# Optimization experiments

Hardware: AMD Instinct MI355X
Metric: run time of the kernel (lower is better)

Reference implementation:

```python
import jax, jax.numpy as jnp
import numpy as np

D_MODEL = 1024
D_STATE = 128


def setup_inputs() -> dict:
    key = jax.random.key(0)
    ks = jax.random.split(key, 16)
    dm, ds = D_MODEL, D_STATE
    def lin(kw, kb, out_f, in_f):
        # torch nn.Linear default init: U(-1/sqrt(in), 1/sqrt(in))
        bound = 1.0 / np.sqrt(in_f)
        W = jax.random.uniform(kw, (out_f, in_f), jnp.float32, -bound, bound)
        b = jax.random.uniform(kb, (out_f,), jnp.float32, -bound, bound)
        return W, b
    x = jax.random.normal(ks[0], (8, 2048, dm), jnp.float32)
    A = jax.random.normal(ks[1], (ds, ds), jnp.float32) * 0.05  # scaled for stability of the recurrence
    B_w, B_b = lin(ks[2], ks[3], ds, dm)
    C_w, C_b = lin(ks[4], ks[5], dm, ds)
    D_w, D_b = lin(ks[6], ks[7], dm, dm)
    s_w1, s_b1 = lin(ks[8], ks[9], dm // 2, dm)
    s_w2, s_b2 = lin(ks[10], ks[11], ds, dm // 2)
    g_w, g_b = lin(ks[12], ks[13], dm, dm)
    return {"x": x, "A": A, "B_w": B_w, "B_b": B_b, "C_w": C_w, "C_b": C_b,
            "D_w": D_w, "D_b": D_b, "s_w1": s_w1, "s_b1": s_b1,
            "s_w2": s_w2, "s_b2": s_b2, "g_w": g_w, "g_b": g_b}


def reference(x, A, B_w, B_b, C_w, C_b, D_w, D_b, s_w1, s_b1, s_w2, s_b2, g_w, g_b):
    # Precompute all per-timestep input projections as batched GEMMs.
    s = jax.nn.sigmoid(jax.nn.silu(jnp.einsum('btd,hd->bth', x, s_w1) + s_b1)
                       @ s_w2.T + s_b2)            # [B,T,d_state] selection gate
    Bt = jnp.einsum('btd,sd->bts', x, B_w) + B_b    # [B,T,d_state]
    u = Bt * s                                      # driving input to the recurrence

    # Linear recurrence h_t = h_{t-1} @ A.T + u_t via lax.scan over time.
    h0 = jnp.zeros((x.shape[0], A.shape[0]), x.dtype)
    def step(h, u_t):
        h = h @ A.T + u_t
        return h, h
    _, hs = jax.lax.scan(step, h0, jnp.swapaxes(u, 0, 1))  # [T,B,d_state]
    hs = jnp.swapaxes(hs, 0, 1)                            # [B,T,d_state]

    y = jnp.einsum('bts,ds->btd', hs, C_w) + C_b + jnp.einsum('btd,ed->bte', x, D_w) + D_b
    gate = jax.nn.sigmoid(jnp.einsum('btd,ed->bte', x, g_w) + g_b)
    return y * gate
```

## Files before the change

kernel.cpp:

```cpp
#include <hip/hip_runtime.h>
#include <hip/hip_bf16.h>

typedef __bf16 bf16x8 __attribute__((ext_vector_type(8)));
typedef float f32x4 __attribute__((ext_vector_type(4)));

#define M_TOK 16384
#define CHUNK 64
#define NCHUNK 32

__device__ __forceinline__ void gload16(const void* g, void* l) {
    __builtin_amdgcn_global_load_lds(
        (const __attribute__((address_space(1))) void*)g,
        (__attribute__((address_space(3))) void*)l, 16, 0, 0);
}

__device__ __forceinline__ float sigmoidf_(float v) { return 1.f / (1.f + __expf(-v)); }

__global__ __launch_bounds__(256) void f32_to_bf16_k(const float* __restrict__ in,
                                                     __hip_bfloat16* __restrict__ out, int n8) {
    int i = blockIdx.x * 256 + threadIdx.x;
    if (i >= n8) return;
    const f32x4* p4 = reinterpret_cast<const f32x4*>(in) + (size_t)i * 2;
    f32x4 a = p4[0], b = p4[1];
    union { __hip_bfloat16 h[8]; uint4 u; } o;
    o.h[0] = __float2bfloat16(a[0]); o.h[1] = __float2bfloat16(a[1]);
    o.h[2] = __float2bfloat16(a[2]); o.h[3] = __float2bfloat16(a[3]);
    o.h[4] = __float2bfloat16(b[0]); o.h[5] = __float2bfloat16(b[1]);
    o.h[6] = __float2bfloat16(b[2]); o.h[7] = __float2bfloat16(b[3]);
    *reinterpret_cast<uint4*>(out + (size_t)i * 8) = o.u;
}

__global__ __launch_bounds__(256)
void wconv6(const float* s0, const float* s1, const float* s2, const float* s3,
            const float* s4, const float* s5,
            __hip_bfloat16* d0, __hip_bfloat16* d1, __hip_bfloat16* d2,
            __hip_bfloat16* d3, __hip_bfloat16* d4, __hip_bfloat16* d5,
            int n0, int n1, int n2, int n3, int n4, int n5) {
    const float* src; __hip_bfloat16* dst; int n8;
    switch (blockIdx.y) {
        case 0: src = s0; dst = d0; n8 = n0; break;
        case 1: src = s1; dst = d1; n8 = n1; break;
        case 2: src = s2; dst = d2; n8 = n2; break;
        case 3: src = s3; dst = d3; n8 = n3; break;
        case 4: src = s4; dst = d4; n8 = n4; break;
        default: src = s5; dst = d5; n8 = n5; break;
    }
    int i = blockIdx.x * 256 + threadIdx.x;
    if (i >= n8) return;
    const f32x4* p4 = reinterpret_cast<const f32x4*>(src) + (size_t)i * 2;
    f32x4 a = p4[0], b = p4[1];
    union { __hip_bfloat16 h[8]; uint4 u; } o;
    o.h[0] = __float2bfloat16(a[0]); o.h[1] = __float2bfloat16(a[1]);
    o.h[2] = __float2bfloat16(a[2]); o.h[3] = __float2bfloat16(a[3]);
    o.h[4] = __float2bfloat16(b[0]); o.h[5] = __float2bfloat16(b[1]);
    o.h[6] = __float2bfloat16(b[2]); o.h[7] = __float2bfloat16(b[3]);
    *reinterpret_cast<uint4*>(dst + (size_t)i * 8) = o.u;
}

__device__ __forceinline__ void stage128(const __hip_bfloat16* src, int ldk, size_t row0,
                                         int k0, char* lds, int tid) {
    #pragma unroll
    for (int j = 0; j < 4; ++j) {
        int q = tid + 256 * j;
        int row = q >> 3, c8 = q & 7;
        int cb = (c8 * 16) ^ ((row & 7) << 4);
        gload16((const char*)(src + (row0 + row) * (size_t)ldk + k0) + cb, lds + q * 16);
    }
}

template<int MODE>
__global__ __launch_bounds__(256, 2)
void gemm128(const __hip_bfloat16* __restrict__ X, const __hip_bfloat16* __restrict__ W,
             const __hip_bfloat16* __restrict__ Gw, const __hip_bfloat16* __restrict__ HS,
             const __hip_bfloat16* __restrict__ CW,
             const float* __restrict__ bias, const float* __restrict__ bias2,
             const float* __restrict__ biasG,
             float* __restrict__ outF, __hip_bfloat16* __restrict__ outB) {
    constexpr int N = (MODE == 0) ? 512 : 1024;
    constexpr int nN = N / 128;
    __shared__ __align__(16) char Xs[16384];
    __shared__ __align__(16) char Ws[16384];
    __shared__ __align__(16) char Gs[(MODE == 1) ? 16384 : 16];

    const int nwg  = gridDim.x;
    const int orig = blockIdx.x;
    const int v    = (orig & 7) * (nwg >> 3) + (orig >> 3);
    const size_t m0 = (size_t)(v / nN) * 128;
    const int    n0 = (v % nN) * 128;
    const int tid = threadIdx.x, lane = tid & 63, wid = tid >> 6;
    const int wm = wid >> 1, wn = wid & 1;
    const int lr = lane & 15, lg = lane >> 4;

    auto frag = [&](const char* base, int R, int kk) -> bf16x8 {
        int cb = (kk * 64 + lg * 16) ^ ((R & 7) << 4);
        return *reinterpret_cast<const bf16x8*>(base + R * 128 + cb);
    };

    f32x4 accY[4][4] = {};
    f32x4 accG[(MODE == 1) ? 4 : 1][4] = {};

    for (int k0 = 0; k0 < 1024; k0 += 64) {
        __syncthreads();
        stage128(X, 1024, m0, k0, Xs, tid);
        stage128(W, 1024, (size_t)n0, k0, Ws, tid);
        if constexpr (MODE == 1) stage128(Gw, 1024, (size_t)n0, k0, Gs, tid);
        __syncthreads();
        #pragma unroll
        for (int kk = 0; kk < 2; ++kk) {
            bf16x8 af[4];
            #pragma unroll
            for (int m = 0; m < 4; ++m) af[m] = frag(Xs, wm*64 + m*16 + lr, kk);
            #pragma unroll
            for (int n = 0; n < 4; ++n) {
                bf16x8 bw = frag(Ws, wn*64 + n*16 + lr, kk);
                #pragma unroll
                for (int m = 0; m < 4; ++m)
                    accY[m][n] = __builtin_amdgcn_mfma_f32_16x16x32_bf16(af[m], bw, accY[m][n], 0, 0, 0);
                if constexpr (MODE == 1) {
                    bf16x8 bg = frag(Gs, wn*64 + n*16 + lr, kk);
                    #pragma unroll
                    for (int m = 0; m < 4; ++m)
                        accG[m][n] = __builtin_amdgcn_mfma_f32_16x16x32_bf16(af[m], bg, accG[m][n], 0, 0, 0);
                }
            }
        }
    }
    if constexpr (MODE == 1) {
        for (int k0 = 0; k0 < 128; k0 += 64) {
            __syncthreads();
            stage128(HS, 128, m0, k0, Xs, tid);
            stage128(CW, 128, (size_t)n0, k0, Ws, tid);
            __syncthreads();
            #pragma unroll
            for (int kk = 0; kk < 2; ++kk) {
                bf16x8 af[4];
                #pragma unroll
                for (int m = 0; m < 4; ++m) af[m] = frag(Xs, wm*64 + m*16 + lr, kk);
                #pragma unroll
                for (int n = 0; n < 4; ++n) {
                    bf16x8 bw = frag(Ws, wn*64 + n*16 + lr, kk);
                    #pragma unroll
                    for (int m = 0; m < 4; ++m)
                        accY[m][n] = __builtin_amdgcn_mfma_f32_16x16x32_bf16(af[m], bw, accY[m][n], 0, 0, 0);
                }
            }
        }
    }

    #pragma unroll
    for (int m = 0; m < 4; ++m)
        #pragma unroll
        for (int n = 0; n < 4; ++n)
            #pragma unroll
            for (int rr = 0; rr < 4; ++rr) {
                size_t row = m0 + wm*64 + m*16 + lg*4 + rr;
                int col = n0 + wn*64 + n*16 + lr;
                if constexpr (MODE == 0) {
                    float vv = accY[m][n][rr] + bias[col];
                    outB[row * N + col] = __float2bfloat16(vv * sigmoidf_(vv));
                } else {
                    float y = accY[m][n][rr] + bias[col] + bias2[col];
                    float g = accG[m][n][rr] + biasG[col];
                    outF[row * 1024 + col] = y * sigmoidf_(g);
                }
            }
}

__global__ __launch_bounds__(256)
void gemm_u(const __hip_bfloat16* __restrict__ Z1, const __hip_bfloat16* __restrict__ W2,
            const float* __restrict__ b2,
            const __hip_bfloat16* __restrict__ X, const __hip_bfloat16* __restrict__ Bw,
            const float* __restrict__ Bb, __hip_bfloat16* __restrict__ U) {
    __shared__ __align__(16) char As[64 * 128];
    __shared__ __align__(16) char Bs[128 * 128];
    const int orig = blockIdx.x;
    const int v = (orig & 7) * 32 + (orig >> 3);
    const int m0 = v * 64;
    const int tid = threadIdx.x;
    const int wid = tid >> 6, lane = tid & 63;
    const int wm = wid >> 1, wn = wid & 1;
    const int lr = lane & 15, lg = lane >> 4;
    const int srow = tid >> 3, sc8 = tid & 7;

    auto fragA = [&](int R, int kk) -> bf16x8 {
        int cb = (kk * 64 + lg * 16) ^ ((R & 7) << 4);
        return *reinterpret_cast<const bf16x8*>(As + R * 128 + cb);
    };
    auto fragB = [&](int R, int kk) -> bf16x8 {
        int cb = (kk * 64 + lg * 16) ^ ((R & 7) << 4);
        return *reinterpret_cast<const bf16x8*>(Bs + R * 128 + cb);
    };

    f32x4 accS[2][4] = {};
    for (int k0 = 0; k0 < 512; k0 += 64) {
        __syncthreads();
        #pragma unroll
        for (int j = 0; j < 2; ++j) {
            int row = srow + j * 32, q = tid + 256 * j;
            int cb = (sc8 * 16) ^ ((row & 7) << 4);
            gload16((const char*)&Z1[(size_t)(m0 + row) * 512 + k0] + cb, As + q * 16);
        }
        #pragma unroll
        for (int j = 0; j < 4; ++j) {
            int row = srow + j * 32, q = tid + 256 * j;
            int cb = (sc8 * 16) ^ ((row & 7) << 4);
            gload16((const char*)&W2[(size_t)row * 512 + k0] + cb, Bs + q * 16);
        }
        __syncthreads();
        #pragma unroll
        for (int kk = 0; kk < 2; ++kk) {
            bf16x8 af[2], bfr[4];
            #pragma unroll
            for (int m = 0; m < 2; ++m) af[m] = fragA(wm*32 + m*16 + lr, kk);
            #pragma unroll
            for (int n = 0; n < 4; ++n) bfr[n] = fragB(wn*64 + n*16 + lr, kk);
            #pragma unroll
            for (int m = 0; m < 2; ++m)
                #pragma unroll
                for (int n = 0; n < 4; ++n)
                    accS[m][n] = __builtin_amdgcn_mfma_f32_16x16x32_bf16(af[m], bfr[n], accS[m][n], 0, 0, 0);
        }
    }
    #pragma unroll
    for (int m = 0; m < 2; ++m)
        #pragma unroll
        for (int n = 0; n < 4; ++n)
            #pragma unroll
            for (int r = 0; r < 4; ++r) {
                int col = wn*64 + n*16 + lr;
                accS[m][n][r] = sigmoidf_(accS[m][n][r] + b2[col]);
            }
    f32x4 accU[2][4] = {};
    for (int k0 = 0; k0 < 1024; k0 += 64) {
        __syncthreads();
        #pragma unroll
        for (int j = 0; j < 2; ++j) {
            int row = srow + j * 32, q = tid + 256 * j;
            int cb = (sc8 * 16) ^ ((row & 7) << 4);
            gload16((const char*)&X[(size_t)(m0 + row) * 1024 + k0] + cb, As + q * 16);
        }
        #pragma unroll
        for (int j = 0; j < 4; ++j) {
            int row = srow + j * 32, q = tid + 256 * j;
            int cb = (sc8 * 16) ^ ((row & 7) << 4);
            gload16((const char*)&Bw[(size_t)row * 1024 + k0] + cb, Bs + q * 16);
        }
        __syncthreads();
        #pragma unroll
        for (int kk = 0; kk < 2; ++kk) {
            bf16x8 af[2], bfr[4];
            #pragma unroll
            for (int m = 0; m < 2; ++m) af[m] = fragA(wm*32 + m*16 + lr, kk);
            #pragma unroll
            for (int n = 0; n < 4; ++n) bfr[n] = fragB(wn*64 + n*16 + lr, kk);
            #pragma unroll
            for (int m = 0; m < 2; ++m)
                #pragma unroll
                for (int n = 0; n < 4; ++n)
                    accU[m][n] = __builtin_amdgcn_mfma_f32_16x16x32_bf16(af[m], bfr[n], accU[m][n], 0, 0, 0);
        }
    }
    #pragma unroll
    for (int m = 0; m < 2; ++m)
        #pragma unroll
        for (int n = 0; n < 4; ++n)
            #pragma unroll
            for (int r = 0; r < 4; ++r) {
                int row = m0 + wm*32 + m*16 + lg*4 + r;
                int col = wn*64 + n*16 + lr;
                float uval = (accU[m][n][r] + Bb[col]) * accS[m][n][r];
                U[(size_t)row * 128 + col] = __float2bfloat16(uval);
            }
}

__global__ __launch_bounds__(128) void matpow8(const float* __restrict__ P,
                                               float* __restrict__ O) {
    __shared__ float Pl[128 * 132];
    __shared__ __align__(16) float v[2][128];
    const int tid = threadIdx.x, j = blockIdx.x;
    #pragma unroll 8
    for (int r = 0; r < 128; ++r) Pl[r * 132 + tid] = P[r * 128 + tid];
    v[0][tid] = P[tid * 128 + j];
    __syncthreads();
    int cur = 0;
    for (int it = 0; it < 7; ++it) {
        const f32x4* row = reinterpret_cast<const f32x4*>(&Pl[tid * 132]);
        const f32x4* hv  = reinterpret_cast<const f32x4*>(v[cur]);
        f32x4 s4 = {0.f, 0.f, 0.f, 0.f};
        #pragma unroll
        for (int k = 0; k < 32; ++k) s4 += row[k] * hv[k];
        v[cur ^ 1][tid] = s4[0] + s4[1] + s4[2] + s4[3];
        __syncthreads();
        cur ^= 1;
    }
    O[tid * 128 + j] = v[cur][tid];
}

__global__ __launch_bounds__(128) void ssm_phase1(const float* __restrict__ A,
                                                  const __hip_bfloat16* __restrict__ u,
                                                  float* __restrict__ E) {
    __shared__ float Al[128 * 132];
    __shared__ __align__(16) float hbuf[2][128];
    const int tid = threadIdx.x;
    #pragma unroll 8
    for (int r = 0; r < 128; ++r) Al[r * 132 + tid] = A[r * 128 + tid];
    hbuf[0][tid] = 0.f;
    __syncthreads();
    const int b = blockIdx.x >> 5, c = blockIdx.x & 31;
    const __hip_bfloat16* up = u + ((size_t)b * 2048 + c * CHUNK) * 128;
    const f32x4* Arow = reinterpret_cast<const f32x4*>(&Al[tid * 132]);
    int cur = 0;
    for (int t = 0; t < CHUNK; ++t) {
        const f32x4* hv = reinterpret_cast<const f32x4*>(hbuf[cur]);
        f32x4 s4 = {0.f, 0.f, 0.f, 0.f};
        #pragma unroll
        for (int k = 0; k < 32; ++k) s4 += Arow[k] * hv[k];
        float val = s4[0] + s4[1] + s4[2] + s4[3] + __bfloat162float(up[t * 128 + tid]);
        hbuf[cur ^ 1][tid] = val;
        __syncthreads();
        cur ^= 1;
    }
    E[(size_t)blockIdx.x * 128 + tid] = hbuf[cur][tid];
}

__global__ __launch_bounds__(128) void ssm_phase2(const float* __restrict__ A64,
                                                  const float* __restrict__ E,
                                                  float* __restrict__ starts) {
    __shared__ float Al[128 * 132];
    __shared__ __align__(16) float st[2][128];
    const int tid = threadIdx.x;
    const int b = blockIdx.x;
    #pragma unroll 8
    for (int r = 0; r < 128; ++r) Al[r * 132 + tid] = A64[r * 128 + tid];
    st[0][tid] = 0.f;
    __syncthreads();
    const f32x4* Arow = reinterpret_cast<const f32x4*>(&Al[tid * 132]);
    int cur = 0;
    for (int c = 0; c < NCHUNK; ++c) {
        starts[((size_t)b * NCHUNK + c) * 128 + tid] = st[cur][tid];
        const f32x4* hv = reinterpret_cast<const f32x4*>(st[cur]);
        f32x4 s4 = {0.f, 0.f, 0.f, 0.f};
        #pragma unroll
        for (int k = 0; k < 32; ++k) s4 += Arow[k] * hv[k];
        float val = s4[0] + s4[1] + s4[2] + s4[3] + E[((size_t)b * NCHUNK + c) * 128 + tid];
        st[cur ^ 1][tid] = val;
        __syncthreads();
        cur ^= 1;
    }
}

__global__ __launch_bounds__(128) void ssm_phase3(const float* __restrict__ A,
                                                  const __hip_bfloat16* __restrict__ u,
                                                  const float* __restrict__ starts,
                                                  __hip_bfloat16* __restrict__ hs) {
    __shared__ float Al[128 * 132];
    __shared__ __align__(16) float hbuf[2][128];
    const int tid = threadIdx.x;
    #pragma unroll 8
    for (int r = 0; r < 128; ++r) Al[r * 132 + tid] = A[r * 128 + tid];
    hbuf[0][tid] = starts[(size_t)blockIdx.x * 128 + tid];
    __syncthreads();
    const int b = blockIdx.x >> 5, c = blockIdx.x & 31;
    const size_t tok0 = (size_t)b * 2048 + c * CHUNK;
    const __hip_bfloat16* up = u + tok0 * 128;
    const f32x4* Arow = reinterpret_cast<const f32x4*>(&Al[tid * 132]);
    int cur = 0;
    for (int t = 0; t < CHUNK; ++t) {
        const f32x4* hv = reinterpret_cast<const f32x4*>(hbuf[cur]);
        f32x4 s4 = {0.f, 0.f, 0.f, 0.f};
        #pragma unroll
        for (int k = 0; k < 32; ++k) s4 += Arow[k] * hv[k];
        float val = s4[0] + s4[1] + s4[2] + s4[3] + __bfloat162float(up[t * 128 + tid]);
        hs[(tok0 + t) * 128 + tid] = __float2bfloat16(val);
        hbuf[cur ^ 1][tid] = val;
        __syncthreads();
        cur ^= 1;
    }
}

extern "C" void kernel_launch(void* const* d_in, const int* in_sizes, int n_in,
                              void* d_out, int out_size, void* d_ws, size_t ws_size,
                              hipStream_t stream) {
    const float* x    = (const float*)d_in[0];
    const float* A    = (const float*)d_in[1];
    const float* B_w  = (const float*)d_in[2];
    const float* B_b  = (const float*)d_in[3];
    const float* C_w  = (const float*)d_in[4];
    const float* C_b  = (const float*)d_in[5];
    const float* D_w  = (const float*)d_in[6];
    const float* D_b  = (const float*)d_in[7];
    const float* s_w1 = (const float*)d_in[8];
    const float* s_b1 = (const float*)d_in[9];
    const float* s_w2 = (const float*)d_in[10];
    const float* s_b2 = (const float*)d_in[11];
    const float* g_w  = (const float*)d_in[12];
    const float* g_b  = (const float*)d_in[13];
    float* out = (float*)d_out;

    char* p = (char*)d_ws;
    auto alloc = [&](size_t n) { char* r = p; p += (n + 255) & ~(size_t)255; return r; };
    __hip_bfloat16* xb    = (__hip_bfloat16*)alloc((size_t)M_TOK * 1024 * 2);
    __hip_bfloat16* w1b   = (__hip_bfloat16*)alloc(512 * 1024 * 2);
    __hip_bfloat16* w2b   = (__hip_bfloat16*)alloc(128 * 512 * 2);
    __hip_bfloat16* Bwb   = (__hip_bfloat16*)alloc(128 * 1024 * 2);
    __hip_bfloat16* Cwb   = (__hip_bfloat16*)alloc(1024 * 128 * 2);
    __hip_bfloat16* Dwb   = (__hip_bfloat16*)alloc(1024 * 1024 * 2);
    __hip_bfloat16* gwb   = (__hip_bfloat16*)alloc(1024 * 1024 * 2);
    __hip_bfloat16* z1b   = (__hip_bfloat16*)alloc((size_t)M_TOK * 512 * 2);
    __hip_bfloat16* ub    = (__hip_bfloat16*)alloc((size_t)M_TOK * 128 * 2);
    __hip_bfloat16* hsb   = (__hip_bfloat16*)alloc((size_t)M_TOK * 128 * 2);
    float* pa       = (float*)alloc(128 * 128 * 4);
    float* pb       = (float*)alloc(128 * 128 * 4);
    float* Ebuf     = (float*)alloc(256 * 128 * 4);
    float* startbuf = (float*)alloc(256 * 128 * 4);

    matpow8<<<128, 128, 0, stream>>>(A,  pa);
    matpow8<<<128, 128, 0, stream>>>(pa, pb);

    f32_to_bf16_k<<<dim3((M_TOK * 1024 / 8 + 255) / 256), dim3(256), 0, stream>>>(
        x, xb, M_TOK * 1024 / 8);
    wconv6<<<dim3(512, 6), dim3(256), 0, stream>>>(
        s_w1, s_w2, B_w, C_w, D_w, g_w,
        w1b, w2b, Bwb, Cwb, Dwb, gwb,
        512 * 1024 / 8, 128 * 512 / 8, 128 * 1024 / 8, 1024 * 128 / 8,
        1024 * 1024 / 8, 1024 * 1024 / 8);

    gemm128<0><<<dim3(512), dim3(256), 0, stream>>>(
        xb, w1b, nullptr, nullptr, nullptr, s_b1, nullptr, nullptr, nullptr, z1b);
    gemm_u<<<dim3(256), dim3(256), 0, stream>>>(z1b, w2b, s_b2, xb, Bwb, B_b, ub);

    ssm_phase1<<<256, 128, 0, stream>>>(A, ub, Ebuf);
    ssm_phase2<<<8, 128, 0, stream>>>(pb, Ebuf, startbuf);
    ssm_phase3<<<256, 128, 0, stream>>>(A, ub, startbuf, hsb);

    gemm128<1><<<dim3(1024), dim3(256), 0, stream>>>(
        xb, Dwb, gwb, hsb, Cwb, D_b, C_b, g_b, out, nullptr);
}
```

Measured before the change: 239.4 us.

## Keep transition matrix rows in registers and prefetch chunk inputs into LDS

Each thread of the scan, state-passing and matrix-power kernels now holds its row of A in 128 VGPRs instead of re-reading it from a padded LDS copy every step. The chunk's u inputs (or E values) are bulk-prefetched into LDS up front rather than loaded from global memory on every timestep. The dot product is also split into four independent accumulators to shorten the serial FMA dependency chain. The costs are very high register pressure (launch_bounds 128,1) and a slightly different summation order.

```diff
diff --git a/kernel.cpp b/kernel.cpp
--- a/kernel.cpp
+++ b/kernel.cpp
@@ -273,106 +273,138 @@
             }
 }
 
-__global__ __launch_bounds__(128) void matpow8(const float* __restrict__ P,
-                                               float* __restrict__ O) {
-    __shared__ float Pl[128 * 132];
+__global__ __launch_bounds__(128, 1) void matpow8(const float* __restrict__ P,
+                                                  float* __restrict__ O) {
     __shared__ __align__(16) float v[2][128];
-    const int tid = threadIdx.x, j = blockIdx.x;
-    #pragma unroll 8
-    for (int r = 0; r < 128; ++r) Pl[r * 132 + tid] = P[r * 128 + tid];
-    v[0][tid] = P[tid * 128 + j];
+    const int tid = threadIdx.x, col = blockIdx.x;
+    f32x4 pr[32];
+    #pragma unroll
+    for (int k = 0; k < 32; ++k) pr[k] = *reinterpret_cast<const f32x4*>(&P[tid * 128 + k * 4]);
+    v[0][tid] = P[tid * 128 + col];
     __syncthreads();
     int cur = 0;
     for (int it = 0; it < 7; ++it) {
-        const f32x4* row = reinterpret_cast<const f32x4*>(&Pl[tid * 132]);
-        const f32x4* hv  = reinterpret_cast<const f32x4*>(v[cur]);
-        f32x4 s4 = {0.f, 0.f, 0.f, 0.f};
-        #pragma unroll
-        for (int k = 0; k < 32; ++k) s4 += row[k] * hv[k];
-        v[cur ^ 1][tid] = s4[0] + s4[1] + s4[2] + s4[3];
+        const f32x4* hv = reinterpret_cast<const f32x4*>(v[cur]);
+        f32x4 s0{}, s1{}, s2{}, s3{};
+        #pragma unroll
+        for (int k = 0; k < 32; k += 4) {
+            s0 += pr[k]     * hv[k];
+            s1 += pr[k + 1] * hv[k + 1];
+            s2 += pr[k + 2] * hv[k + 2];
+            s3 += pr[k + 3] * hv[k + 3];
+        }
+        f32x4 ss = (s0 + s1) + (s2 + s3);
+        v[cur ^ 1][tid] = ss[0] + ss[1] + ss[2] + ss[3];
         __syncthreads();
         cur ^= 1;
     }
-    O[tid * 128 + j] = v[cur][tid];
-}
-
-__global__ __launch_bounds__(128) void ssm_phase1(const float* __restrict__ A,
-                                                  const __hip_bfloat16* __restrict__ u,
-                                                  float* __restrict__ E) {
-    __shared__ float Al[128 * 132];
-    __shared__ __align__(16) float hbuf[2][128];
+    O[tid * 128 + col] = v[cur][tid];
+}
+
+__global__ __launch_bounds__(128, 1) void ssm_phase1(const float* __restrict__ A,
+                                                     const __hip_bfloat16* __restrict__ u,
+                                                     float* __restrict__ E) {
+    __shared__ __align__(16) float hb[2][128];
+    __shared__ __align__(16) __hip_bfloat16 uL[CHUNK * 128];
     const int tid = threadIdx.x;
-    #pragma unroll 8
-    for (int r = 0; r < 128; ++r) Al[r * 132 + tid] = A[r * 128 + tid];
-    hbuf[0][tid] = 0.f;
-    __syncthreads();
+    f32x4 ar[32];
+    #pragma unroll
+    for (int k = 0; k < 32; ++k) ar[k] = *reinterpret_cast<const f32x4*>(&A[tid * 128 + k * 4]);
     const int b = blockIdx.x >> 5, c = blockIdx.x & 31;
     const __hip_bfloat16* up = u + ((size_t)b * 2048 + c * CHUNK) * 128;
-    const f32x4* Arow = reinterpret_cast<const f32x4*>(&Al[tid * 132]);
+    #pragma unroll
+    for (int q = 0; q < 8; ++q)
+        gload16(up + ((size_t)(q * 128 + tid)) * 8, &uL[(q * 128 + tid) * 8]);
+    hb[0][tid] = 0.f;
+    __syncthreads();
     int cur = 0;
     for (int t = 0; t < CHUNK; ++t) {
-        const f32x4* hv = reinterpret_cast<const f32x4*>(hbuf[cur]);
-        f32x4 s4 = {0.f, 0.f, 0.f, 0.f};
-        #pragma unroll
-        for (int k = 0; k < 32; ++k) s4 += Arow[k] * hv[k];
-        float val = s4[0] + s4[1] + s4[2] + s4[3] + __bfloat162float(up[t * 128 + tid]);
-        hbuf[cur ^ 1][tid] = val;
+        const f32x4* hv = reinterpret_cast<const f32x4*>(hb[cur]);
+        f32x4 s0{}, s1{}, s2{}, s3{};
+        #pragma unroll
+        for (int k = 0; k < 32; k += 4) {
+            s0 += ar[k]     * hv[k];
+            s1 += ar[k + 1] * hv[k + 1];
+            s2 += ar[k + 2] * hv[k + 2];
+            s3 += ar[k + 3] * hv[k + 3];
+        }
+        f32x4 ss = (s0 + s1) + (s2 + s3);
+        float val = ss[0] + ss[1] + ss[2] + ss[3] + __bfloat162float(uL[t * 128 + tid]);
+        hb[cur ^ 1][tid] = val;
         __syncthreads();
         cur ^= 1;
     }
-    E[(size_t)blockIdx.x * 128 + tid] = hbuf[cur][tid];
-}
-
-__global__ __launch_bounds__(128) void ssm_phase2(const float* __restrict__ A64,
-                                                  const float* __restrict__ E,
-                                                  float* __restrict__ starts) {
-    __shared__ float Al[128 * 132];
+    E[(size_t)blockIdx.x * 128 + tid] = hb[cur][tid];
+}
+
+__global__ __launch_bounds__(128, 1) void ssm_phase2(const float* __restrict__ A64,
+                                                     const float* __restrict__ E,
+                                                     float* __restrict__ starts) {
     __shared__ __align__(16) float st[2][128];
-    const int tid = threadIdx.x;
-    const int b = blockIdx.x;
-    #pragma unroll 8
-    for (int r = 0; r < 128; ++r) Al[r * 132 + tid] = A64[r * 128 + tid];
+    __shared__ __align__(16) float El[NCHUNK * 128];
+    const int tid = threadIdx.x, b = blockIdx.x;
+    f32x4 ar[32];
+    #pragma unroll
+    for (int k = 0; k < 32; ++k) ar[k] = *reinterpret_cast<const f32x4*>(&A64[tid * 128 + k * 4]);
+    const f32x4* Eg = reinterpret_cast<const f32x4*>(E + (size_t)b * NCHUNK * 128);
+    #pragma unroll
+    for (int q = 0; q < 8; ++q)
+        reinterpret_cast<f32x4*>(El)[q * 128 + tid] = Eg[q * 128 + tid];
     st[0][tid] = 0.f;
     __syncthreads();
-    const f32x4* Arow = reinterpret_cast<const f32x4*>(&Al[tid * 132]);
     int cur = 0;
     for (int c = 0; c < NCHUNK; ++c) {
         starts[((size_t)b * NCHUNK + c) * 128 + tid] = st[cur][tid];
         const f32x4* hv = reinterpret_cast<const f32x4*>(st[cur]);
-        f32x4 s4 = {0.f, 0.f, 0.f, 0.f};
-        #pragma unroll
-        for (int k = 0; k < 32; ++k) s4 += Arow[k] * hv[k];
-        float val = s4[0] + s4[1] + s4[2] + s4[3] + E[((size_t)b * NCHUNK + c) * 128 + tid];
+        f32x4 s0{}, s1{}, s2{}, s3{};
+        #pragma unroll
+        for (int k = 0; k < 32; k += 4) {
+            s0 += ar[k]     * hv[k];
+            s1 += ar[k + 1] * hv[k + 1];
+            s2 += ar[k + 2] * hv[k + 2];
+            s3 += ar[k + 3] * hv[k + 3];
+        }
+        f32x4 ss = (s0 + s1) + (s2 + s3);
+        float val = ss[0] + ss[1] + ss[2] + ss[3] + El[c * 128 + tid];
         st[cur ^ 1][tid] = val;
         __syncthreads();
         cur ^= 1;
     }
 }
 
-__global__ __launch_bounds__(128) void ssm_phase3(const float* __restrict__ A,
-                                                  const __hip_bfloat16* __restrict__ u,
-                                                  const float* __restrict__ starts,
-                                                  __hip_bfloat16* __restrict__ hs) {
-    __shared__ float Al[128 * 132];
-    __shared__ __align__(16) float hbuf[2][128];
+__global__ __launch_bounds__(128, 1) void ssm_phase3(const float* __restrict__ A,
+                                                     const __hip_bfloat16* __restrict__ u,
+                                                     const float* __restrict__ starts,
+                                                     __hip_bfloat16* __restrict__ hs) {
+    __shared__ __align__(16) float hb[2][128];
+    __shared__ __align__(16) __hip_bfloat16 uL[CHUNK * 128];
     const int tid = threadIdx.x;
-    #pragma unroll 8
-    for (int r = 0; r < 128; ++r) Al[r * 132 + tid] = A[r * 128 + tid];
-    hbuf[0][tid] = starts[(size_t)blockIdx.x * 128 + tid];
-    __syncthreads();
+    f32x4 ar[32];
+    #pragma unroll
+    for (int k = 0; k < 32; ++k) ar[k] = *reinterpret_cast<const f32x4*>(&A[tid * 128 + k * 4]);
     const int b = blockIdx.x >> 5, c = blockIdx.x & 31;
     const size_t tok0 = (size_t)b * 2048 + c * CHUNK;
     const __hip_bfloat16* up = u + tok0 * 128;
-    const f32x4* Arow = reinterpret_cast<const f32x4*>(&Al[tid * 132]);
+    #pragma unroll
+    for (int q = 0; q < 8; ++q)
+        gload16(up + ((size_t)(q * 128 + tid)) * 8, &uL[(q * 128 + tid) * 8]);
+    hb[0][tid] = starts[(size_t)blockIdx.x * 128 + tid];
+    __syncthreads();
     int cur = 0;
     for (int t = 0; t < CHUNK; ++t) {
-        const f32x4* hv = reinterpret_cast<const f32x4*>(hbuf[cur]);
-        f32x4 s4 = {0.f, 0.f, 0.f, 0.f};
-        #pragma unroll
-        for (int k = 0; k < 32; ++k) s4 += Arow[k] * hv[k];
-        float val = s4[0] + s4[1] + s4[2] + s4[3] + __bfloat162float(up[t * 128 + tid]);
+        const f32x4* hv = reinterpret_cast<const f32x4*>(hb[cur]);
+        f32x4 s0{}, s1{}, s2{}, s3{};
+        #pragma unroll
+        for (int k = 0; k < 32; k += 4) {
+            s0 += ar[k]     * hv[k];
+            s1 += ar[k + 1] * hv[k + 1];
+            s2 += ar[k + 2] * hv[k + 2];
+            s3 += ar[k + 3] * hv[k + 3];
+        }
+        f32x4 ss = (s0 + s1) + (s2 + s3);
+        float val = ss[0] + ss[1] + ss[2] + ss[3] + __bfloat162float(uL[t * 128 + tid]);
         hs[(tok0 + t) * 128 + tid] = __float2bfloat16(val);
-        hbuf[cur ^ 1][tid] = val;
+        hb[cur ^ 1][tid] = val;
         __syncthreads();
         cur ^= 1;
     }
```

Result: faster. 229.4 us (-4.2%).
